# Optimization experiments

Hardware: AMD Instinct MI355X
Metric: run time of the kernel (lower is better)

Reference implementation:

```python
import jax, jax.numpy as jnp
import numpy as np

T, H, F, E, K = 2048, 1024, 1024, 8, 2  # tokens, hidden, ffn, experts, top_k


def setup_inputs() -> dict:
    key = jax.random.key(0)
    k1, k2, k3, k4, k5 = jax.random.split(key, 5)
    hidden_states = jax.random.normal(k1, (T, H), dtype=jnp.float32)
    # router outputs: positive weights (renormalize=False in module, used as-is)
    topk_weights = jax.random.uniform(k2, (T, K), dtype=jnp.float32)
    topk_ids = jax.random.randint(k3, (T, K), 0, E, dtype=jnp.int32)
    # gate_up: (E, 2F, H) with first F rows = gate, last F rows = up
    gate_up_weight = jax.random.normal(k4, (E, 2 * F, H), dtype=jnp.float32) * 0.02
    # down: (E, H, F)
    down_weight = jax.random.normal(k5, (E, H, F), dtype=jnp.float32) * 0.02
    return {
        'hidden_states': hidden_states,
        'topk_weights': topk_weights,
        'topk_ids': topk_ids,
        'gate_up_weight': gate_up_weight,
        'down_weight': down_weight,
    }


def reference(hidden_states, topk_weights, topk_ids, gate_up_weight, down_weight):
    # Fused MoE: per selected expert, y = (silu(x@Wg^T) * (x@Wu^T)) @ Wd^T,
    # combined with router weights (renormalize=False).
    f = down_weight.shape[-1]
    # [T, E, 2F]: gate_up projection for every expert (dense ref for grouped GEMM)
    gu = jnp.einsum('th,eoh->teo', hidden_states, gate_up_weight)
    gate, up = gu[..., :f], gu[..., f:]
    act = jax.nn.silu(gate) * up                     # [T, E, F]
    y = jnp.einsum('tef,ehf->teh', act, down_weight)  # [T, E, H]
    # gather the top-k experts per token and combine
    y_sel = jnp.take_along_axis(y, topk_ids[:, :, None], axis=1)  # [T, K, H]
    out = jnp.sum(y_sel * topk_weights[:, :, None], axis=1)       # [T, H]
    return out.astype(hidden_states.dtype)
```

## Files before the change

### kernel.cpp

```cpp
#include <hip/hip_runtime.h>
#include <hip/hip_bf16.h>

#define T_TOK 2048
#define HID   1024
#define FF    1024
#define NEXP  8
#define NPAIR 4096

#define BM 128
#define BK 32
#define MAX_MT 40
#define MAXROWS (MAX_MT*BM)
#define PPT (NPAIR/256)

using bf16x8 = __attribute__((ext_vector_type(8))) __bf16;
using f32x4  = __attribute__((ext_vector_type(4))) float;

__device__ __forceinline__ unsigned short f2bf(float f) {
    unsigned int u = __float_as_uint(f);
    return (unsigned short)((u + 0x7FFF + ((u >> 16) & 1)) >> 16);
}
__device__ __forceinline__ float bf2f(unsigned short s) {
    return __uint_as_float(((unsigned int)s) << 16);
}
__device__ __forceinline__ void gll16(const unsigned short* g, unsigned short* l) {
    __builtin_amdgcn_global_load_lds(
        (const __attribute__((address_space(1))) void*)(const void*)g,
        (__attribute__((address_space(3))) void*)(void*)l, 16, 0, 0);
}
__device__ __forceinline__ ushort4 cvt4(float4 v) {
    ushort4 o; o.x = f2bf(v.x); o.y = f2bf(v.y); o.z = f2bf(v.z); o.w = f2bf(v.w);
    return o;
}

#define B_WGU 2048
#define B_WDN 1024
#define B_HS  256
#define B_TOT (B_WGU + B_WDN + B_HS)

__global__ void prep_kernel(const float* __restrict__ wgu,
                            const float* __restrict__ wdn,
                            const float* __restrict__ hs,
                            const int* __restrict__ ids,
                            int* __restrict__ pair_pos,
                            int* __restrict__ row_tok,
                            int* __restrict__ meta,
                            unsigned short* __restrict__ wgu_b,
                            unsigned short* __restrict__ wdn_b,
                            unsigned short* __restrict__ hs_b) {
    int tid = threadIdx.x;
    int bid = blockIdx.x;
    if (bid < B_TOT) {
        const float4* src;
        ushort4* dst;
        long base;
        if (bid < B_WGU) {
            src = (const float4*)wgu; dst = (ushort4*)wgu_b;
            base = (long)bid * 2048 + tid;
        } else if (bid < B_WGU + B_WDN) {
            src = (const float4*)wdn; dst = (ushort4*)wdn_b;
            base = (long)(bid - B_WGU) * 2048 + tid;
        } else {
            src = (const float4*)hs; dst = (ushort4*)hs_b;
            base = (long)(bid - B_WGU - B_WDN) * 2048 + tid;
        }
        float4 v[8];
#pragma unroll
        for (int k = 0; k < 8; k++) v[k] = src[base + k * 256];
#pragma unroll
        for (int k = 0; k < 8; k++) dst[base + k * 256] = cvt4(v[k]);
        return;
    }
    __shared__ int S[2][256][NEXP];
    __shared__ int base[NEXP];
    int myc[NEXP];
    int eloc[PPT];
#pragma unroll
    for (int e = 0; e < NEXP; e++) myc[e] = 0;
#pragma unroll
    for (int i = 0; i < PPT; i++) {
        int e = ids[tid * PPT + i];
        eloc[i] = e;
#pragma unroll
        for (int ee = 0; ee < NEXP; ee++) myc[ee] += (e == ee);
    }
#pragma unroll
    for (int e = 0; e < NEXP; e++) S[0][tid][e] = myc[e];
    __syncthreads();
    int src = 0;
    for (int d = 1; d < 256; d <<= 1) {
#pragma unroll
        for (int e = 0; e < NEXP; e++) {
            int v = S[src][tid][e];
            if (tid >= d) v += S[src][tid - d][e];
            S[src ^ 1][tid][e] = v;
        }
        __syncthreads();
        src ^= 1;
    }
    if (tid == 0) {
        int mt = 0;
        for (int e = 0; e < NEXP; e++) {
            meta[e] = mt;
            base[e] = mt * BM;
            mt += (S[src][255][e] + BM - 1) / BM;
        }
        meta[NEXP] = mt;
    }
    for (int i = tid; i < MAXROWS; i += 256) row_tok[i] = -1;
    __syncthreads();
    int off[NEXP];
#pragma unroll
    for (int e = 0; e < NEXP; e++) off[e] = base[e] + S[src][tid][e] - myc[e];
#pragma unroll
    for (int i = 0; i < PPT; i++) {
        int p = tid * PPT + i;
        int e = eloc[i];
        int pos = 0;
#pragma unroll
        for (int ee = 0; ee < NEXP; ee++) if (e == ee) pos = off[ee]++;
        pair_pos[p] = pos;
        row_tok[pos] = p >> 1;
    }
}

template<int EPI, int NBY, int BN>
__global__ __launch_bounds__(256)
void gemm_moe(const unsigned short* __restrict__ A,
              const unsigned short* __restrict__ B,
              unsigned short* __restrict__ Cbf,
              const int* __restrict__ meta,
              const int* __restrict__ row_tok,
              int K, long Bexp) {
    constexpr int NJ = BN / 32;
    constexpr int ACH = (BM * BK) / (8 * 256);
    constexpr int NBCH = (BN * BK) / (8 * 256);
    static_assert(ACH + NBCH == 4, "vmcnt immediates assume 4 loads per stage");
    __shared__ unsigned short As[3][BM * BK];
    __shared__ unsigned short Bs[3][BN * BK];

    int tid = threadIdx.x;
    int L = blockIdx.x;
    int xcd = L & 7;
    int slot = L >> 3;
    constexpr int PER = NBY / 8;
    int by = xcd * PER + (slot % PER);
    int bx = slot / PER;
    if (bx >= meta[NEXP]) return;
    int e = 0;
#pragma unroll
    for (int i = 1; i < NEXP; i++) if (bx >= meta[i]) e = i;

    long m0 = (long)bx * BM;
    int n0 = by * BN;
    const unsigned short* Bb = B + (long)e * Bexp;

    int lane = tid & 63, wv = tid >> 6;
    const int r = lane & 15;
    const int q = lane >> 4;
    const int mw = (wv >> 1) * 64, nw = (wv & 1) * (BN / 2);
    const int sw = (q ^ ((r >> 1) & 3)) * 8;

    const unsigned short* ap[ACH];
#pragma unroll
    for (int h = 0; h < ACH; h++) {
        int c = h * 256 + tid;
        int row = c >> 2, cp = c & 3;
        int cc = cp ^ ((row >> 1) & 3);
        long grow;
        if (EPI == 1) {
            int tk = row_tok[m0 + row];
            if (tk < 0) tk = 0;
            grow = tk;
        } else {
            grow = m0 + row;
        }
        ap[h] = A + grow * (long)K + cc * 8;
    }
    const unsigned short* bp[NBCH];
#pragma unroll
    for (int h = 0; h < NBCH; h++) {
        int c = h * 256 + tid;
        int row = c >> 2, cp = c & 3;
        int cc = cp ^ ((row >> 1) & 3);
        long grow;
        if (EPI == 1) grow = ((row & 1) ? FF : 0) + ((n0 + row) >> 1);
        else          grow = n0 + row;
        bp[h] = Bb + grow * (long)K + cc * 8;
    }

    auto stage = [&](int s, int k0) {
#pragma unroll
        for (int h = 0; h < ACH; h++)
            gll16(ap[h] + k0, &As[s][(h * 256 + tid) * 8]);
#pragma unroll
        for (int h = 0; h < NBCH; h++)
            gll16(bp[h] + k0, &Bs[s][(h * 256 + tid) * 8]);
    };

    f32x4 acc[4][NJ] = {};
    const int NKI = K / BK;
    stage(0, 0);
    stage(1, BK);
    int sb = 0;
    for (int ki = 0; ki < NKI; ki++) {
        if (ki + 1 < NKI) asm volatile("s_waitcnt vmcnt(4)" ::: "memory");
        else              asm volatile("s_waitcnt vmcnt(0)" ::: "memory");
        __builtin_amdgcn_s_barrier();
        __builtin_amdgcn_sched_barrier(0);
        if (ki + 2 < NKI) {
            int sn = sb + 2; if (sn >= 3) sn -= 3;
            stage(sn, (ki + 2) * BK);
        }
        bf16x8 a[4], b[NJ];
#pragma unroll
        for (int i = 0; i < 4; i++)
            a[i] = *(const bf16x8*)&As[sb][(mw + i * 16 + r) * BK + sw];
#pragma unroll
        for (int j = 0; j < NJ; j++)
            b[j] = *(const bf16x8*)&Bs[sb][(nw + j * 16 + r) * BK + sw];
#pragma unroll
        for (int i = 0; i < 4; i++)
#pragma unroll
            for (int j = 0; j < NJ; j++)
                acc[i][j] = __builtin_amdgcn_mfma_f32_16x16x32_bf16(a[i], b[j], acc[i][j], 0, 0, 0);
        sb = (sb == 2) ? 0 : sb + 1;
    }

    if (EPI == 1) {
#pragma unroll
        for (int i = 0; i < 4; i++) {
            long rowb = m0 + mw + i * 16 + q * 4;
#pragma unroll
            for (int j = 0; j < NJ; j++) {
                int n = n0 + nw + j * 16 + r;
#pragma unroll
                for (int reg = 0; reg < 4; reg++) {
                    float v = acc[i][j][reg];
                    float o = __shfl_xor(v, 1);
                    if (!(r & 1)) {
                        float g = v, u = o;
                        float s2 = g / (1.f + __expf(-g)) * u;
                        Cbf[(rowb + reg) * (long)FF + (n >> 1)] = f2bf(s2);
                    }
                }
            }
        }
    } else {
#pragma unroll
        for (int i = 0; i < 4; i++) {
            long rowb = m0 + mw + i * 16 + q * 4;
#pragma unroll
            for (int j = 0; j < NJ; j++) {
                int n = n0 + nw + j * 16 + r;
#pragma unroll
                for (int reg = 0; reg < 4; reg++)
                    Cbf[(rowb + reg) * (long)HID + n] = f2bf(acc[i][j][reg]);
            }
        }
    }
}

__global__ void combine_kernel(const unsigned short* __restrict__ y,
                               const float* __restrict__ tw,
                               const int* __restrict__ pair_pos,
                               float* __restrict__ out) {
    int t = blockIdx.x;
    int c = threadIdx.x * 4;
    int p0 = pair_pos[t * 2], p1 = pair_pos[t * 2 + 1];
    float w0 = tw[t * 2], w1 = tw[t * 2 + 1];
    ushort4 a = *(const ushort4*)(y + (long)p0 * HID + c);
    ushort4 b = *(const ushort4*)(y + (long)p1 * HID + c);
    float4 o;
    o.x = w0 * bf2f(a.x) + w1 * bf2f(b.x);
    o.y = w0 * bf2f(a.y) + w1 * bf2f(b.y);
    o.z = w0 * bf2f(a.z) + w1 * bf2f(b.z);
    o.w = w0 * bf2f(a.w) + w1 * bf2f(b.w);
    *(float4*)(out + (long)t * HID + c) = o;
}

extern "C" void kernel_launch(void* const* d_in, const int* in_sizes, int n_in,
                              void* d_out, int out_size, void* d_ws, size_t ws_size,
                              hipStream_t stream) {
    const float* hs  = (const float*)d_in[0];
    const float* tw  = (const float*)d_in[1];
    const int*   ids = (const int*)d_in[2];
    const float* wgu = (const float*)d_in[3];
    const float* wdn = (const float*)d_in[4];
    float* out = (float*)d_out;

    char* ws = (char*)d_ws;
    size_t off = 0;
    auto alloc = [&](size_t bytes) -> void* {
        void* p = ws + off;
        off += (bytes + 255) & ~(size_t)255;
        return p;
    };
    unsigned short* wgu_b = (unsigned short*)alloc((size_t)NEXP * 2 * FF * HID * 2);
    unsigned short* wdn_b = (unsigned short*)alloc((size_t)NEXP * HID * FF * 2);
    unsigned short* hs_b  = (unsigned short*)alloc((size_t)T_TOK * HID * 2);
    unsigned short* act   = (unsigned short*)alloc((size_t)MAXROWS * FF * 2);
    unsigned short* ybuf  = (unsigned short*)alloc((size_t)MAXROWS * HID * 2);
    int* pair_pos = (int*)alloc(NPAIR * 4);
    int* row_tok  = (int*)alloc(MAXROWS * 4);
    int* meta     = (int*)alloc(64);

    prep_kernel<<<B_TOT + 1, 256, 0, stream>>>(wgu, wdn, hs, ids,
                                               pair_pos, row_tok, meta,
                                               wgu_b, wdn_b, hs_b);

    gemm_moe<1, 16, 128><<<16 * MAX_MT, 256, 0, stream>>>(
        hs_b, wgu_b, act, meta, row_tok, HID, (long)(2 * FF) * HID);

    gemm_moe<2, 8, 128><<<8 * MAX_MT, 256, 0, stream>>>(
        act, wdn_b, ybuf, meta, row_tok, FF, (long)HID * FF);

    combine_kernel<<<T_TOK, 256, 0, stream>>>(ybuf, tw, pair_pos, out);
}
```

Measured before the change: 207.5 us.

## Split GEMM K dimension across two wave teams with LDS reduction

The MoE GEMM kernel now launches 512 threads as two teams of four waves. Each team processes half of the K range with its own double-buffered LDS tiles, and team 1's partial accumulators are reduced through LDS into team 0 before the epilogue. This replaces the 3-stage vmcnt-tuned pipeline with a simpler __syncthreads double buffer. The down-projection launch moves to BN=64 with twice as many N blocks, and the prep conversion now writes 16-byte vector stores. The aim is more waves per tile to hide latency and more blocks for the second GEMM, at the cost of extra barriers, reduction traffic and a less aggressive prefetch.

New measurement: 219.4 us. 1.06x slower.

```diff
diff --git a/kernel.cpp b/kernel.cpp
--- a/kernel.cpp
+++ b/kernel.cpp
@@ -15,6 +15,7 @@
 
 using bf16x8 = __attribute__((ext_vector_type(8))) __bf16;
 using f32x4  = __attribute__((ext_vector_type(4))) float;
+using us8    = __attribute__((ext_vector_type(8))) unsigned short;
 
 __device__ __forceinline__ unsigned short f2bf(float f) {
     unsigned int u = __float_as_uint(f);
@@ -52,23 +53,27 @@
     int bid = blockIdx.x;
     if (bid < B_TOT) {
         const float4* src;
-        ushort4* dst;
-        long base;
-        if (bid < B_WGU) {
-            src = (const float4*)wgu; dst = (ushort4*)wgu_b;
-            base = (long)bid * 2048 + tid;
-        } else if (bid < B_WGU + B_WDN) {
-            src = (const float4*)wdn; dst = (ushort4*)wdn_b;
-            base = (long)(bid - B_WGU) * 2048 + tid;
-        } else {
-            src = (const float4*)hs; dst = (ushort4*)hs_b;
-            base = (long)(bid - B_WGU - B_WDN) * 2048 + tid;
-        }
+        us8* dst;
+        long rel;
+        if (bid < B_WGU)            { src = (const float4*)wgu; dst = (us8*)wgu_b; rel = bid; }
+        else if (bid < B_WGU+B_WDN) { src = (const float4*)wdn; dst = (us8*)wdn_b; rel = bid - B_WGU; }
+        else                        { src = (const float4*)hs;  dst = (us8*)hs_b;  rel = bid - B_WGU - B_WDN; }
+        long f4 = rel * 2048 + tid * 2;
         float4 v[8];
 #pragma unroll
-        for (int k = 0; k < 8; k++) v[k] = src[base + k * 256];
-#pragma unroll
-        for (int k = 0; k < 8; k++) dst[base + k * 256] = cvt4(v[k]);
+        for (int k = 0; k < 4; k++) {
+            v[2 * k]     = src[f4 + k * 512];
+            v[2 * k + 1] = src[f4 + k * 512 + 1];
+        }
+        long u8i = rel * 1024 + tid;
+#pragma unroll
+        for (int k = 0; k < 4; k++) {
+            ushort4 lo = cvt4(v[2 * k]), hi = cvt4(v[2 * k + 1]);
+            us8 o;
+            o[0] = lo.x; o[1] = lo.y; o[2] = lo.z; o[3] = lo.w;
+            o[4] = hi.x; o[5] = hi.y; o[6] = hi.z; o[7] = hi.w;
+            dst[u8i + k * 256] = o;
+        }
         return;
     }
     __shared__ int S[2][256][NEXP];
@@ -125,19 +130,22 @@
 }
 
 template<int EPI, int NBY, int BN>
-__global__ __launch_bounds__(256)
+__global__ __launch_bounds__(512)
 void gemm_moe(const unsigned short* __restrict__ A,
               const unsigned short* __restrict__ B,
               unsigned short* __restrict__ Cbf,
               const int* __restrict__ meta,
               const int* __restrict__ row_tok,
               int K, long Bexp) {
-    constexpr int NJ = BN / 32;
+    constexpr int BN2 = BN / 2;
+    constexpr int NJ  = BN / 32;
     constexpr int ACH = (BM * BK) / (8 * 256);
-    constexpr int NBCH = (BN * BK) / (8 * 256);
-    static_assert(ACH + NBCH == 4, "vmcnt immediates assume 4 loads per stage");
-    __shared__ unsigned short As[3][BM * BK];
-    __shared__ unsigned short Bs[3][BN * BK];
+    constexpr int BCH = (BN * BK) / (8 * 256);
+    constexpr int ABYTES = 2 * 2 * BM * BK * 2;
+    constexpr int BBYTES = 2 * 2 * BN * BK * 2;
+    __shared__ __align__(16) unsigned char smem[ABYTES + BBYTES];
+    unsigned short* Asm = (unsigned short*)smem;
+    unsigned short* Bsm = (unsigned short*)(smem + ABYTES);
 
     int tid = threadIdx.x;
     int L = blockIdx.x;
@@ -156,15 +164,18 @@
     const unsigned short* Bb = B + (long)e * Bexp;
 
     int lane = tid & 63, wv = tid >> 6;
+    int team = wv >> 2, wq = wv & 3;
+    int t256 = tid & 255;
     const int r = lane & 15;
     const int q = lane >> 4;
-    const int mw = (wv >> 1) * 64, nw = (wv & 1) * (BN / 2);
+    const int mw = (wq >> 1) * 64, nw = (wq & 1) * BN2;
     const int sw = (q ^ ((r >> 1) & 3)) * 8;
+    const int kbase = team * (K / 2);
 
     const unsigned short* ap[ACH];
 #pragma unroll
     for (int h = 0; h < ACH; h++) {
-        int c = h * 256 + tid;
+        int c = h * 256 + t256;
         int row = c >> 2, cp = c & 3;
         int cc = cp ^ ((row >> 1) & 3);
         long grow;
@@ -175,57 +186,75 @@
         } else {
             grow = m0 + row;
         }
-        ap[h] = A + grow * (long)K + cc * 8;
-    }
-    const unsigned short* bp[NBCH];
-#pragma unroll
-    for (int h = 0; h < NBCH; h++) {
-        int c = h * 256 + tid;
+        ap[h] = A + grow * (long)K + kbase + cc * 8;
+    }
+    const unsigned short* bp[BCH];
+#pragma unroll
+    for (int h = 0; h < BCH; h++) {
+        int c = h * 256 + t256;
         int row = c >> 2, cp = c & 3;
         int cc = cp ^ ((row >> 1) & 3);
         long grow;
         if (EPI == 1) grow = ((row & 1) ? FF : 0) + ((n0 + row) >> 1);
         else          grow = n0 + row;
-        bp[h] = Bb + grow * (long)K + cc * 8;
-    }
-
+        bp[h] = Bb + grow * (long)K + kbase + cc * 8;
+    }
+
+    auto AS = [&](int s) { return Asm + (s * 2 + team) * (BM * BK); };
+    auto BS = [&](int s) { return Bsm + (s * 2 + team) * (BN * BK); };
     auto stage = [&](int s, int k0) {
 #pragma unroll
         for (int h = 0; h < ACH; h++)
-            gll16(ap[h] + k0, &As[s][(h * 256 + tid) * 8]);
-#pragma unroll
-        for (int h = 0; h < NBCH; h++)
-            gll16(bp[h] + k0, &Bs[s][(h * 256 + tid) * 8]);
+            gll16(ap[h] + k0, &AS(s)[(h * 256 + t256) * 8]);
+#pragma unroll
+        for (int h = 0; h < BCH; h++)
+            gll16(bp[h] + k0, &BS(s)[(h * 256 + t256) * 8]);
     };
 
     f32x4 acc[4][NJ] = {};
-    const int NKI = K / BK;
+    const int NKI = K / (2 * BK);
     stage(0, 0);
-    stage(1, BK);
-    int sb = 0;
     for (int ki = 0; ki < NKI; ki++) {
-        if (ki + 1 < NKI) asm volatile("s_waitcnt vmcnt(4)" ::: "memory");
-        else              asm volatile("s_waitcnt vmcnt(0)" ::: "memory");
-        __builtin_amdgcn_s_barrier();
-        __builtin_amdgcn_sched_barrier(0);
-        if (ki + 2 < NKI) {
-            int sn = sb + 2; if (sn >= 3) sn -= 3;
-            stage(sn, (ki + 2) * BK);
-        }
+        __syncthreads();
+        if (ki + 1 < NKI) stage((ki + 1) & 1, (ki + 1) * BK);
+        int s = ki & 1;
+        const unsigned short* as_ = AS(s);
+        const unsigned short* bs_ = BS(s);
         bf16x8 a[4], b[NJ];
 #pragma unroll
         for (int i = 0; i < 4; i++)
-            a[i] = *(const bf16x8*)&As[sb][(mw + i * 16 + r) * BK + sw];
+            a[i] = *(const bf16x8*)&as_[(mw + i * 16 + r) * BK + sw];
 #pragma unroll
         for (int j = 0; j < NJ; j++)
-            b[j] = *(const bf16x8*)&Bs[sb][(nw + j * 16 + r) * BK + sw];
+            b[j] = *(const bf16x8*)&bs_[(nw + j * 16 + r) * BK + sw];
 #pragma unroll
         for (int i = 0; i < 4; i++)
 #pragma unroll
             for (int j = 0; j < NJ; j++)
                 acc[i][j] = __builtin_amdgcn_mfma_f32_16x16x32_bf16(a[i], b[j], acc[i][j], 0, 0, 0);
-        sb = (sb == 2) ? 0 : sb + 1;
-    }
+        __syncthreads();
+    }
+
+    float* red = (float*)smem;
+    float* wr = red + wq * (64 * BN2);
+    if (team == 1) {
+#pragma unroll
+        for (int i = 0; i < 4; i++)
+#pragma unroll
+            for (int j = 0; j < NJ; j++)
+#pragma unroll
+                for (int reg = 0; reg < 4; reg++)
+                    wr[(i * 16 + q * 4 + reg) * BN2 + j * 16 + r] = acc[i][j][reg];
+    }
+    __syncthreads();
+    if (team == 1) return;
+#pragma unroll
+    for (int i = 0; i < 4; i++)
+#pragma unroll
+        for (int j = 0; j < NJ; j++)
+#pragma unroll
+            for (int reg = 0; reg < 4; reg++)
+                acc[i][j][reg] += wr[(i * 16 + q * 4 + reg) * BN2 + j * 16 + r];
 
     if (EPI == 1) {
 #pragma unroll
@@ -309,10 +338,10 @@
                                                pair_pos, row_tok, meta,
                                                wgu_b, wdn_b, hs_b);
 
-    gemm_moe<1, 16, 128><<<16 * MAX_MT, 256, 0, stream>>>(
+    gemm_moe<1, 16, 128><<<16 * MAX_MT, 512, 0, stream>>>(
         hs_b, wgu_b, act, meta, row_tok, HID, (long)(2 * FF) * HID);
 
-    gemm_moe<2, 8, 128><<<8 * MAX_MT, 256, 0, stream>>>(
+    gemm_moe<2, 16, 64><<<16 * MAX_MT, 512, 0, stream>>>(
         act, wdn_b, ybuf, meta, row_tok, FF, (long)HID * FF);
 
     combine_kernel<<<T_TOK, 256, 0, stream>>>(ybuf, tw, pair_pos, out);
```
